# Kernel optimization log

Hardware: AMD Instinct MI355X
Metric: run time of the kernel (lower is better)

Reference implementation:

```python
import jax, jax.numpy as jnp
import numpy as np

NEG_INF = -1e10  # matches torch -10000000000.0


def setup_inputs() -> dict:
    key = jax.random.key(0)
    ks = jax.random.split(key, 8)
    L, B, E, H, HID, A = 2048, 32, 512, 512, 512, 512
    input_data = jax.random.normal(ks[0], (L, B, E), dtype=jnp.float32)
    mask = jax.random.randint(ks[1], (L, B), 0, 2, dtype=jnp.int32)
    action_feature = jax.random.normal(ks[2], (B, A), dtype=jnp.float32)
    hidden_state = jax.random.normal(ks[3], (B, H), dtype=jnp.float32)
    state = jax.random.normal(ks[4], (B, H), dtype=jnp.float32)
    W1 = jax.random.normal(ks[5], (H + E, HID), dtype=jnp.float32) * (1.0 / np.sqrt(H + E))
    b1 = jnp.zeros((HID,), dtype=jnp.float32)
    W2 = jax.random.normal(ks[6], (HID, 1), dtype=jnp.float32) * (1.0 / np.sqrt(HID))
    b2 = jnp.zeros((1,), dtype=jnp.float32)
    return {"input_data": input_data, "mask": mask, "action_feature": action_feature,
            "hidden_state": hidden_state, "state": state,
            "W1": W1, "b1": b1, "W2": W2, "b2": b2}


def reference(input_data, mask, action_feature, hidden_state, state, W1, b1, W2, b2):
    # input_data: (L, B, E); hidden_state: (B, H)
    H = hidden_state.shape[-1]
    # query = concat([hidden broadcast over L, input_data], -1); split W1 to avoid
    # materializing the (L, B, H+E) concat.
    W1_h, W1_e = W1[:H], W1[H:]                      # (H, HID), (E, HID)
    pre = hidden_state @ W1_h + b1                   # (B, HID)
    pre = pre[None] + jnp.einsum('lbe,eh->lbh', input_data, W1_e)  # (L, B, HID)
    logit = (jnp.tanh(pre) @ W2).squeeze(-1) + b2[0]  # (L, B)
    logit = jnp.where(mask != 0, logit, NEG_INF)
    p = jax.nn.softmax(logit, axis=0)                 # softmax over L
    ctx = jnp.einsum('lbe,lb->be', input_data, p)     # (B, E)
    return jnp.concatenate([ctx, action_feature], axis=1)
```

## Files before the change

### kernel.cpp

```cpp
#include <hip/hip_runtime.h>
#include <hip/hip_bf16.h>
#include <stdint.h>

#define L_DIM 2048
#define B_DIM 32
#define E_DIM 512
#define HID_DIM 512
#define M_DIM (L_DIM * B_DIM)

typedef float f32x4 __attribute__((ext_vector_type(4)));
typedef short bf16x8 __attribute__((ext_vector_type(8)));

#define OFF_BASE  0
#define OFF_WT    65536
#define OFF_LOGIT 589824
#define OFF_P     851968
#define OFF_PART  1114112

__device__ __forceinline__ unsigned short f2bf(float f) {
  unsigned int u = __float_as_uint(f);
  u = (u + 0x7FFFu + ((u >> 16) & 1u)) >> 16;
  return (unsigned short)u;
}

__device__ __forceinline__ float tanh_fast(float x) {
  float xc = fminf(fmaxf(x, -15.f), 15.f);
  float e = __expf(2.f * xc);
  return (e - 1.f) * __builtin_amdgcn_rcpf(e + 1.f);
}

__global__ __launch_bounds__(256) void k_base(const float* __restrict__ hidden,
                                              const float* __restrict__ W1,
                                              const float* __restrict__ b1,
                                              float* __restrict__ base) {
  const int b = blockIdx.x;
  const int tid = threadIdx.x;
  __shared__ float hs[HID_DIM];
  {
    float2 v = *(const float2*)(hidden + (size_t)b * 512 + tid * 2);
    hs[tid * 2] = v.x; hs[tid * 2 + 1] = v.y;
  }
  __syncthreads();
  const int h = tid * 2;
  float2 b1v = *(const float2*)(b1 + h);
  float ax = b1v.x, ay = b1v.y;
#pragma unroll 8
  for (int e = 0; e < 512; ++e) {
    float2 w = *(const float2*)(W1 + (size_t)e * 512 + h);
    float hv = hs[e];
    ax = fmaf(hv, w.x, ax);
    ay = fmaf(hv, w.y, ay);
  }
  float2 r; r.x = ax; r.y = ay;
  *(float2*)(base + (size_t)b * 512 + h) = r;
}

__global__ __launch_bounds__(256) void k_prep_wt(const float* __restrict__ W1,
                                                 unsigned short* __restrict__ Wt) {
  const int kc = blockIdx.x;
  const int tid = threadIdx.x;
  __shared__ unsigned short sh[32][516];
#pragma unroll
  for (int i = 0; i < 16; ++i) {
    int f4 = i * 256 + tid;
    int r = f4 >> 7;
    int c = (f4 & 127) * 4;
    float4 v = *(const float4*)(W1 + (size_t)(512 + kc * 32 + r) * 512 + c);
    sh[r][c + 0] = f2bf(v.x); sh[r][c + 1] = f2bf(v.y);
    sh[r][c + 2] = f2bf(v.z); sh[r][c + 3] = f2bf(v.w);
  }
  __syncthreads();
#pragma unroll
  for (int i = 0; i < 8; ++i) {
    int u = i * 256 + tid;
    int n = ((u >> 9) << 7) + (((u >> 6) & 7) << 4) + (u & 15);
    int k0 = ((u >> 4) & 3) << 3;
    alignas(16) unsigned short tmp[8];
#pragma unroll
    for (int j = 0; j < 8; ++j) tmp[j] = sh[k0 + j][n];
    *(uint4*)(Wt + ((size_t)kc * 2048 + u) * 8) = *(const uint4*)tmp;
  }
}

__global__ __launch_bounds__(512, 4) void k_logits(
    const float* __restrict__ x, const unsigned short* __restrict__ Wt,
    const float* __restrict__ base, const float* __restrict__ W2,
    float* __restrict__ logit) {
  __shared__ unsigned short xs[2][2048];
  const int tid = threadIdx.x;
  const int m0 = blockIdx.x * 64;
  const int w = tid >> 6, lane = tid & 63;
  const int lg = lane >> 4, l15 = lane & 15;

  const int row = tid >> 3, seg4 = tid & 7;
  const int seg8 = seg4 >> 1, half = seg4 & 1;
  const float* xsrc = x + (size_t)(m0 + row) * 512 + seg4 * 4;
  const int xsu = ((row >> 4) * 64 + seg8 * 16 + (row & 15)) * 8 + half * 4;

  int ub[4];
#pragma unroll
  for (int ni = 0; ni < 4; ++ni) {
    int nb = w * 64 + ni * 16;
    ub[ni] = ((nb >> 7) << 9) + (((nb >> 4) & 7) << 6);
  }

  {
    float4 v = *(const float4*)xsrc;
    uint2 pk;
    pk.x = (unsigned)f2bf(v.x) | ((unsigned)f2bf(v.y) << 16);
    pk.y = (unsigned)f2bf(v.z) | ((unsigned)f2bf(v.w) << 16);
    *(uint2*)(&xs[0][xsu]) = pk;
  }
  __syncthreads();

  f32x4 acc[4][4];
#pragma unroll
  for (int mi = 0; mi < 4; ++mi)
#pragma unroll
    for (int ni = 0; ni < 4; ++ni) acc[mi][ni] = (f32x4){0.f, 0.f, 0.f, 0.f};

  for (int kc = 0; kc < 16; ++kc) {
    const int cur = kc & 1;
    uint4 bw[4];
    const uint4* bsrc = (const uint4*)Wt + (size_t)kc * 2048;
#pragma unroll
    for (int ni = 0; ni < 4; ++ni) bw[ni] = bsrc[ub[ni] + lane];
    float4 nx;
    if (kc < 15) nx = *(const float4*)(xsrc + (kc + 1) * 32);
    bf16x8 af[4];
#pragma unroll
    for (int mi = 0; mi < 4; ++mi)
      af[mi] = *(const bf16x8*)(&xs[cur][(mi * 64 + lane) * 8]);
#pragma unroll
    for (int mi = 0; mi < 4; ++mi)
#pragma unroll
      for (int ni = 0; ni < 4; ++ni)
        acc[mi][ni] = __builtin_amdgcn_mfma_f32_16x16x32_bf16(
            af[mi], *(const bf16x8*)(&bw[ni]), acc[mi][ni], 0, 0, 0);
    if (kc < 15) {
      uint2 pk;
      pk.x = (unsigned)f2bf(nx.x) | ((unsigned)f2bf(nx.y) << 16);
      pk.y = (unsigned)f2bf(nx.z) | ((unsigned)f2bf(nx.w) << 16);
      *(uint2*)(&xs[cur ^ 1][xsu]) = pk;
    }
    __syncthreads();
  }

  float w2v[4];
#pragma unroll
  for (int ni = 0; ni < 4; ++ni) w2v[ni] = W2[w * 64 + ni * 16 + l15];
  float lsum[4][4];
#pragma unroll
  for (int mi = 0; mi < 4; ++mi) {
#pragma unroll
    for (int rg = 0; rg < 4; ++rg) {
      int m = m0 + mi * 16 + lg * 4 + rg;
      int bb = m & 31;
      const float* brow = base + (size_t)bb * 512 + w * 64;
      float s = 0.f;
#pragma unroll
      for (int ni = 0; ni < 4; ++ni) {
        float pre = acc[mi][ni][rg] + brow[ni * 16 + l15];
        s = fmaf(tanh_fast(pre), w2v[ni], s);
      }
      lsum[mi][rg] = s;
    }
  }
  float (*lred)[64] = (float (*)[64])xs;
#pragma unroll
  for (int mi = 0; mi < 4; ++mi)
#pragma unroll
    for (int rg = 0; rg < 4; ++rg) {
      float v = lsum[mi][rg];
      v += __shfl_xor(v, 1); v += __shfl_xor(v, 2);
      v += __shfl_xor(v, 4); v += __shfl_xor(v, 8);
      if (l15 == 0) lred[w][mi * 16 + lg * 4 + rg] = v;
    }
  __syncthreads();
  if (tid < 64) {
    float v = 0.f;
#pragma unroll
    for (int wq = 0; wq < 8; ++wq) v += lred[wq][tid];
    logit[m0 + tid] = v;
  }
}

__global__ __launch_bounds__(256) void k_softmax(const float* __restrict__ logit,
                                                 const int* __restrict__ mask,
                                                 float* __restrict__ p) {
  const int b = blockIdx.x, tid = threadIdx.x;
  float lv[8]; float mx = -3.0e38f;
#pragma unroll
  for (int i = 0; i < 8; ++i) {
    int idx = (tid + i * 256) * 32 + b;
    float v = (mask[idx] != 0) ? logit[idx] : -1.0e10f;
    lv[i] = v; mx = fmaxf(mx, v);
  }
  __shared__ float red[8];
  for (int d = 1; d < 64; d <<= 1) mx = fmaxf(mx, __shfl_xor(mx, d));
  if ((tid & 63) == 0) red[tid >> 6] = mx;
  __syncthreads();
  mx = fmaxf(fmaxf(red[0], red[1]), fmaxf(red[2], red[3]));
  float s = 0.f;
#pragma unroll
  for (int i = 0; i < 8; ++i) { lv[i] = __expf(lv[i] - mx); s += lv[i]; }
  for (int d = 1; d < 64; d <<= 1) s += __shfl_xor(s, d);
  __syncthreads();
  if ((tid & 63) == 0) red[4 + (tid >> 6)] = s;
  __syncthreads();
  s = (red[4] + red[5]) + (red[6] + red[7]);
  float inv = 1.f / s;
#pragma unroll
  for (int i = 0; i < 8; ++i) {
    int idx = (tid + i * 256) * 32 + b;
    p[idx] = lv[i] * inv;
  }
}

__global__ __launch_bounds__(128) void k_ctx(const float* __restrict__ x,
                                             const float* __restrict__ p,
                                             float* __restrict__ part) {
  const int blk = blockIdx.x;
  const int b = blk >> 5, ch = blk & 31;
  const int tid = threadIdx.x;
  __shared__ float ps[64];
  const int l0 = ch * 64;
  if (tid < 64) ps[tid] = p[(l0 + tid) * 32 + b];
  __syncthreads();
  const float* xb = x + ((size_t)l0 * 32 + b) * 512 + tid * 4;
  float ax = 0.f, ay = 0.f, az = 0.f, aw = 0.f;
#pragma unroll 4
  for (int i = 0; i < 64; ++i) {
    float4 v = *(const float4*)(xb + (size_t)i * 32 * 512);
    float pv = ps[i];
    ax = fmaf(pv, v.x, ax); ay = fmaf(pv, v.y, ay);
    az = fmaf(pv, v.z, az); aw = fmaf(pv, v.w, aw);
  }
  float4 r; r.x = ax; r.y = ay; r.z = az; r.w = aw;
  *(float4*)(part + (size_t)blk * 512 + tid * 4) = r;
}

__global__ __launch_bounds__(256) void k_final(const float* __restrict__ part,
                                               const float* __restrict__ af,
                                               float* __restrict__ out) {
  const int b = blockIdx.x, tid = threadIdx.x;
  float ax = 0.f, ay = 0.f;
#pragma unroll
  for (int ch = 0; ch < 32; ++ch) {
    float2 v = *(const float2*)(part + ((size_t)(b * 32 + ch) * 512) + tid * 2);
    ax += v.x; ay += v.y;
  }
  float2 r; r.x = ax; r.y = ay;
  *(float2*)(out + (size_t)b * 1024 + tid * 2) = r;
  float2 a = *(const float2*)(af + (size_t)b * 512 + tid * 2);
  *(float2*)(out + (size_t)b * 1024 + 512 + tid * 2) = a;
}

extern "C" void kernel_launch(void* const* d_in, const int* in_sizes, int n_in,
                              void* d_out, int out_size, void* d_ws, size_t ws_size,
                              hipStream_t stream) {
  const float* x      = (const float*)d_in[0];
  const int*   mask   = (const int*)d_in[1];
  const float* af     = (const float*)d_in[2];
  const float* hidden = (const float*)d_in[3];
  const float* W1     = (const float*)d_in[5];
  const float* b1     = (const float*)d_in[6];
  const float* W2     = (const float*)d_in[7];
  float* out = (float*)d_out;
  char* ws = (char*)d_ws;
  float*          base  = (float*)(ws + OFF_BASE);
  unsigned short* Wt    = (unsigned short*)(ws + OFF_WT);
  float*          logit = (float*)(ws + OFF_LOGIT);
  float*          p     = (float*)(ws + OFF_P);
  float*          part  = (float*)(ws + OFF_PART);

  k_base   <<<32,   256, 0, stream>>>(hidden, W1, b1, base);
  k_prep_wt<<<16,   256, 0, stream>>>(W1, Wt);
  k_logits <<<1024, 512, 0, stream>>>(x, Wt, base, W2, logit);
  k_softmax<<<32,   256, 0, stream>>>(logit, mask, p);
  k_ctx    <<<1024, 128, 0, stream>>>(x, p, part);
  k_final  <<<32,   256, 0, stream>>>(part, af, out);
}
```

Before: 107.3 us.

## Stage full 64x512 X tile in LDS up front, drop per-k-step barriers

k_logits now loads and converts the block's entire 64-row X tile to bf16 into 64KB of shared memory before the K loop, instead of double-buffering one 32-wide K chunk per iteration. The K loop then needs no __syncthreads and is unrolled by 2, so MFMA work runs without a block barrier every step. In exchange LDS use per block rises from 8KB to 64KB, which limits how many blocks fit per CU (the launch bounds ask for 4), and global load latency is no longer hidden behind compute. A barrier is added before the shared buffer is reused for the reduction.

```diff
diff --git a/kernel.cpp b/kernel.cpp
--- a/kernel.cpp
+++ b/kernel.cpp
@@ -27,6 +27,15 @@
   float xc = fminf(fmaxf(x, -15.f), 15.f);
   float e = __expf(2.f * xc);
   return (e - 1.f) * __builtin_amdgcn_rcpf(e + 1.f);
+}
+
+__device__ __forceinline__ uint4 pack8(const float4& a, const float4& b) {
+  uint4 r;
+  r.x = (unsigned)f2bf(a.x) | ((unsigned)f2bf(a.y) << 16);
+  r.y = (unsigned)f2bf(a.z) | ((unsigned)f2bf(a.w) << 16);
+  r.z = (unsigned)f2bf(b.x) | ((unsigned)f2bf(b.y) << 16);
+  r.w = (unsigned)f2bf(b.z) | ((unsigned)f2bf(b.w) << 16);
+  return r;
 }
 
 __global__ __launch_bounds__(256) void k_base(const float* __restrict__ hidden,
@@ -86,16 +95,26 @@
     const float* __restrict__ x, const unsigned short* __restrict__ Wt,
     const float* __restrict__ base, const float* __restrict__ W2,
     float* __restrict__ logit) {
-  __shared__ unsigned short xs[2][2048];
+  __shared__ unsigned short xs[32768];
   const int tid = threadIdx.x;
   const int m0 = blockIdx.x * 64;
   const int w = tid >> 6, lane = tid & 63;
   const int lg = lane >> 4, l15 = lane & 15;
 
-  const int row = tid >> 3, seg4 = tid & 7;
-  const int seg8 = seg4 >> 1, half = seg4 & 1;
-  const float* xsrc = x + (size_t)(m0 + row) * 512 + seg4 * 4;
-  const int xsu = ((row >> 4) * 64 + seg8 * 16 + (row & 15)) * 8 + half * 4;
+  {
+    const int r = tid >> 3, j = tid & 7;
+    const float* xrow = x + (size_t)(m0 + r) * 512;
+    const int ubase = ((r >> 4) << 6) + (r & 15);
+#pragma unroll
+    for (int i = 0; i < 8; ++i) {
+      int s = i * 8 + j;
+      float4 a0 = *(const float4*)(xrow + s * 8);
+      float4 a1 = *(const float4*)(xrow + s * 8 + 4);
+      int u = ((s >> 2) << 8) + ((s & 3) << 4) + ubase;
+      *(uint4*)(&xs[u * 8]) = pack8(a0, a1);
+    }
+  }
+  __syncthreads();
 
   int ub[4];
 #pragma unroll
@@ -104,46 +123,28 @@
     ub[ni] = ((nb >> 7) << 9) + (((nb >> 4) & 7) << 6);
   }
 
-  {
-    float4 v = *(const float4*)xsrc;
-    uint2 pk;
-    pk.x = (unsigned)f2bf(v.x) | ((unsigned)f2bf(v.y) << 16);
-    pk.y = (unsigned)f2bf(v.z) | ((unsigned)f2bf(v.w) << 16);
-    *(uint2*)(&xs[0][xsu]) = pk;
-  }
-  __syncthreads();
-
   f32x4 acc[4][4];
 #pragma unroll
   for (int mi = 0; mi < 4; ++mi)
 #pragma unroll
     for (int ni = 0; ni < 4; ++ni) acc[mi][ni] = (f32x4){0.f, 0.f, 0.f, 0.f};
 
+#pragma unroll 2
   for (int kc = 0; kc < 16; ++kc) {
-    const int cur = kc & 1;
     uint4 bw[4];
     const uint4* bsrc = (const uint4*)Wt + (size_t)kc * 2048;
 #pragma unroll
     for (int ni = 0; ni < 4; ++ni) bw[ni] = bsrc[ub[ni] + lane];
-    float4 nx;
-    if (kc < 15) nx = *(const float4*)(xsrc + (kc + 1) * 32);
     bf16x8 af[4];
 #pragma unroll
     for (int mi = 0; mi < 4; ++mi)
-      af[mi] = *(const bf16x8*)(&xs[cur][(mi * 64 + lane) * 8]);
+      af[mi] = *(const bf16x8*)(&xs[(kc * 256 + mi * 64 + lane) * 8]);
 #pragma unroll
     for (int mi = 0; mi < 4; ++mi)
 #pragma unroll
       for (int ni = 0; ni < 4; ++ni)
         acc[mi][ni] = __builtin_amdgcn_mfma_f32_16x16x32_bf16(
             af[mi], *(const bf16x8*)(&bw[ni]), acc[mi][ni], 0, 0, 0);
-    if (kc < 15) {
-      uint2 pk;
-      pk.x = (unsigned)f2bf(nx.x) | ((unsigned)f2bf(nx.y) << 16);
-      pk.y = (unsigned)f2bf(nx.z) | ((unsigned)f2bf(nx.w) << 16);
-      *(uint2*)(&xs[cur ^ 1][xsu]) = pk;
-    }
-    __syncthreads();
   }
 
   float w2v[4];
@@ -166,6 +167,7 @@
       lsum[mi][rg] = s;
     }
   }
+  __syncthreads();
   float (*lred)[64] = (float (*)[64])xs;
 #pragma unroll
   for (int mi = 0; mi < 4; ++mi)
```

Result: slower. 111.3 us (+3.7%).

## Double the logits tile to 128 rows and software-pipeline weight loads

Applied to the files above, without the earlier changes.

The logits GEMM kernel now uses 1024-thread blocks covering 128 rows. Two row groups of waves share each weight fragment load, halving weight traffic per row. Weight fragments are prefetched one k-step ahead into registers through inline global_load asm with explicit vmcnt waits, and the MFMA section runs at raised wave priority. The larger tile and extra prefetch registers raise register pressure under launch_bounds(1024,4), which may cause spills or lower occupancy.

```diff
diff --git a/kernel.cpp b/kernel.cpp
--- a/kernel.cpp
+++ b/kernel.cpp
@@ -10,6 +10,7 @@
 
 typedef float f32x4 __attribute__((ext_vector_type(4)));
 typedef short bf16x8 __attribute__((ext_vector_type(8)));
+typedef unsigned int u32x4 __attribute__((ext_vector_type(4)));
 
 #define OFF_BASE  0
 #define OFF_WT    65536
@@ -28,6 +29,12 @@
   float e = __expf(2.f * xc);
   return (e - 1.f) * __builtin_amdgcn_rcpf(e + 1.f);
 }
+
+#define GLX4(dst, voff, sbase) \
+  asm volatile("global_load_dwordx4 %0, %1, %2" \
+               : "=v"(dst) : "v"(voff), "s"(sbase))
+#define VMWAIT(N) do { asm volatile("s_waitcnt vmcnt(" #N ")" ::: "memory"); \
+                       __builtin_amdgcn_sched_barrier(0); } while (0)
 
 __global__ __launch_bounds__(256) void k_base(const float* __restrict__ hidden,
                                               const float* __restrict__ W1,
@@ -82,81 +89,116 @@
   }
 }
 
-__global__ __launch_bounds__(512, 4) void k_logits(
+__global__ __launch_bounds__(1024, 4) void k_logits(
     const float* __restrict__ x, const unsigned short* __restrict__ Wt,
     const float* __restrict__ base, const float* __restrict__ W2,
     float* __restrict__ logit) {
-  __shared__ unsigned short xs[2][2048];
+  __shared__ unsigned short xs[2][4096];
+  __shared__ float lred[2][8][64];
   const int tid = threadIdx.x;
-  const int m0 = blockIdx.x * 64;
+  const int m0 = blockIdx.x * 128;
   const int w = tid >> 6, lane = tid & 63;
+  const int wm = w >> 3, wn = w & 7;
   const int lg = lane >> 4, l15 = lane & 15;
 
-  const int row = tid >> 3, seg4 = tid & 7;
-  const int seg8 = seg4 >> 1, half = seg4 & 1;
-  const float* xsrc = x + (size_t)(m0 + row) * 512 + seg4 * 4;
-  const int xsu = ((row >> 4) * 64 + seg8 * 16 + (row & 15)) * 8 + half * 4;
-
-  int ub[4];
-#pragma unroll
-  for (int ni = 0; ni < 4; ++ni) {
-    int nb = w * 64 + ni * 16;
-    ub[ni] = ((nb >> 7) << 9) + (((nb >> 4) & 7) << 6);
-  }
+  const int xr = tid >> 3, xseg = tid & 7;
+  const float* xsrc = x + (size_t)(m0 + xr) * 512 + xseg * 4;
+  const int xu8 = (((xr >> 4) << 6) + ((xseg >> 1) << 4) + (xr & 15)) * 8 +
+                  (xseg & 1) * 4;
+
+  unsigned vo[4];
+#pragma unroll
+  for (int ni = 0; ni < 4; ++ni)
+    vo[ni] = ((unsigned)((wn >> 1) * 512 + ((wn & 1) * 4 + ni) * 64 + lane)) * 16u;
+
+  f32x4 acc[4][4];
+#pragma unroll
+  for (int mi = 0; mi < 4; ++mi)
+#pragma unroll
+    for (int ni = 0; ni < 4; ++ni) acc[mi][ni] = (f32x4){0.f, 0.f, 0.f, 0.f};
 
   {
     float4 v = *(const float4*)xsrc;
     uint2 pk;
     pk.x = (unsigned)f2bf(v.x) | ((unsigned)f2bf(v.y) << 16);
     pk.y = (unsigned)f2bf(v.z) | ((unsigned)f2bf(v.w) << 16);
-    *(uint2*)(&xs[0][xsu]) = pk;
-  }
-  __syncthreads();
-
-  f32x4 acc[4][4];
-#pragma unroll
-  for (int mi = 0; mi < 4; ++mi)
-#pragma unroll
-    for (int ni = 0; ni < 4; ++ni) acc[mi][ni] = (f32x4){0.f, 0.f, 0.f, 0.f};
-
-  for (int kc = 0; kc < 16; ++kc) {
+    *(uint2*)(&xs[0][xu8]) = pk;
+  }
+  u32x4 bw[4];
+#pragma unroll
+  for (int ni = 0; ni < 4; ++ni) { GLX4(bw[ni], vo[ni], Wt); vo[ni] += 32768u; }
+  __syncthreads();
+
+#pragma unroll 1
+  for (int kc = 0; kc < 15; ++kc) {
     const int cur = kc & 1;
-    uint4 bw[4];
-    const uint4* bsrc = (const uint4*)Wt + (size_t)kc * 2048;
-#pragma unroll
-    for (int ni = 0; ni < 4; ++ni) bw[ni] = bsrc[ub[ni] + lane];
     float4 nx;
-    if (kc < 15) nx = *(const float4*)(xsrc + (kc + 1) * 32);
+    {
+      unsigned long long xp = (unsigned long long)(xsrc + (kc + 1) * 32);
+      asm volatile("" : "+v"(xp));
+      nx = *(const float4*)xp;
+    }
+    u32x4 bn[4];
+#pragma unroll
+    for (int ni = 0; ni < 4; ++ni) { GLX4(bn[ni], vo[ni], Wt); vo[ni] += 32768u; }
     bf16x8 af[4];
 #pragma unroll
     for (int mi = 0; mi < 4; ++mi)
-      af[mi] = *(const bf16x8*)(&xs[cur][(mi * 64 + lane) * 8]);
+      af[mi] = *(const bf16x8*)(&xs[cur][((wm * 4 + mi) * 64 + lane) * 8]);
+    VMWAIT(5);
+    asm volatile("s_waitcnt lgkmcnt(0)" ::: "memory");
+    __builtin_amdgcn_sched_barrier(0);
+    __builtin_amdgcn_s_setprio(1);
 #pragma unroll
     for (int mi = 0; mi < 4; ++mi)
 #pragma unroll
       for (int ni = 0; ni < 4; ++ni)
         acc[mi][ni] = __builtin_amdgcn_mfma_f32_16x16x32_bf16(
             af[mi], *(const bf16x8*)(&bw[ni]), acc[mi][ni], 0, 0, 0);
-    if (kc < 15) {
+    __builtin_amdgcn_s_setprio(0);
+    VMWAIT(4);
+    {
       uint2 pk;
       pk.x = (unsigned)f2bf(nx.x) | ((unsigned)f2bf(nx.y) << 16);
       pk.y = (unsigned)f2bf(nx.z) | ((unsigned)f2bf(nx.w) << 16);
-      *(uint2*)(&xs[cur ^ 1][xsu]) = pk;
+      *(uint2*)(&xs[cur ^ 1][xu8]) = pk;
     }
+#pragma unroll
+    for (int ni = 0; ni < 4; ++ni) bw[ni] = bn[ni];
     __syncthreads();
   }
-
+  {
+    bf16x8 af[4];
+#pragma unroll
+    for (int mi = 0; mi < 4; ++mi)
+      af[mi] = *(const bf16x8*)(&xs[1][((wm * 4 + mi) * 64 + lane) * 8]);
+    VMWAIT(0);
+    asm volatile("s_waitcnt lgkmcnt(0)" ::: "memory");
+    __builtin_amdgcn_sched_barrier(0);
+#pragma unroll
+    for (int mi = 0; mi < 4; ++mi)
+#pragma unroll
+      for (int ni = 0; ni < 4; ++ni)
+        acc[mi][ni] = __builtin_amdgcn_mfma_f32_16x16x32_bf16(
+            af[mi], *(const bf16x8*)(&bw[ni]), acc[mi][ni], 0, 0, 0);
+  }
+
+  unsigned long long bpi = (unsigned long long)base;
+  unsigned long long wpi = (unsigned long long)W2;
+  asm volatile("" : "+s"(bpi), "+s"(wpi));
+  const float* bp = (const float*)bpi;
+  const float* wp = (const float*)wpi;
   float w2v[4];
 #pragma unroll
-  for (int ni = 0; ni < 4; ++ni) w2v[ni] = W2[w * 64 + ni * 16 + l15];
+  for (int ni = 0; ni < 4; ++ni) w2v[ni] = wp[wn * 64 + ni * 16 + l15];
   float lsum[4][4];
 #pragma unroll
   for (int mi = 0; mi < 4; ++mi) {
 #pragma unroll
     for (int rg = 0; rg < 4; ++rg) {
-      int m = m0 + mi * 16 + lg * 4 + rg;
+      int m = m0 + wm * 64 + mi * 16 + lg * 4 + rg;
       int bb = m & 31;
-      const float* brow = base + (size_t)bb * 512 + w * 64;
+      const float* brow = bp + (size_t)bb * 512 + wn * 64;
       float s = 0.f;
 #pragma unroll
       for (int ni = 0; ni < 4; ++ni) {
@@ -166,7 +208,6 @@
       lsum[mi][rg] = s;
     }
   }
-  float (*lred)[64] = (float (*)[64])xs;
 #pragma unroll
   for (int mi = 0; mi < 4; ++mi)
 #pragma unroll
@@ -174,13 +215,14 @@
       float v = lsum[mi][rg];
       v += __shfl_xor(v, 1); v += __shfl_xor(v, 2);
       v += __shfl_xor(v, 4); v += __shfl_xor(v, 8);
-      if (l15 == 0) lred[w][mi * 16 + lg * 4 + rg] = v;
+      if (l15 == 0) lred[wm][wn][mi * 16 + lg * 4 + rg] = v;
     }
   __syncthreads();
-  if (tid < 64) {
+  if (tid < 128) {
+    const int wmr = tid >> 6, row = tid & 63;
     float v = 0.f;
 #pragma unroll
-    for (int wq = 0; wq < 8; ++wq) v += lred[wq][tid];
+    for (int wq = 0; wq < 8; ++wq) v += lred[wmr][wq][row];
     logit[m0 + tid] = v;
   }
 }
@@ -276,7 +318,7 @@
 
   k_base   <<<32,   256, 0, stream>>>(hidden, W1, b1, base);
   k_prep_wt<<<16,   256, 0, stream>>>(W1, Wt);
-  k_logits <<<1024, 512, 0, stream>>>(x, Wt, base, W2, logit);
+  k_logits <<<512, 1024, 0, stream>>>(x, Wt, base, W2, logit);
   k_softmax<<<32,   256, 0, stream>>>(logit, mask, p);
   k_ctx    <<<1024, 128, 0, stream>>>(x, p, part);
   k_final  <<<32,   256, 0, stream>>>(part, af, out);
```

Measured after the change: 114.3 us. 6.6% more time.

## Stage W1 tiles through double-buffered LDS via async global_load_lds

Applied to the files above, without the earlier changes.

Weight fragments were previously loaded straight from global memory into registers each k-step. Now each block prefetches the next k-chunk of the transposed weight into a double-buffered LDS region using global_load_lds, overlapped with the MFMA work on the current chunk. MFMA sections are also wrapped in s_setprio to favor the math waves. The cost is 64KB of extra LDS per block, which may lower occupancy below the 4-blocks launch bound and reduce latency hiding.

```diff
diff --git a/kernel.cpp b/kernel.cpp
--- a/kernel.cpp
+++ b/kernel.cpp
@@ -28,6 +28,11 @@
   float e = __expf(2.f * xc);
   return (e - 1.f) * __builtin_amdgcn_rcpf(e + 1.f);
 }
+
+#define GLOAD_LDS16(gsrc, ldst) \
+  __builtin_amdgcn_global_load_lds( \
+      (const __attribute__((address_space(1))) void*)(gsrc), \
+      (__attribute__((address_space(3))) void*)(ldst), 16, 0, 0)
 
 __global__ __launch_bounds__(256) void k_base(const float* __restrict__ hidden,
                                               const float* __restrict__ W1,
@@ -86,62 +91,78 @@
     const float* __restrict__ x, const unsigned short* __restrict__ Wt,
     const float* __restrict__ base, const float* __restrict__ W2,
     float* __restrict__ logit) {
-  __shared__ unsigned short xs[2][2048];
+  __shared__ unsigned short bs[2][16384];
+  __shared__ unsigned short xsh[2][2048];
   const int tid = threadIdx.x;
   const int m0 = blockIdx.x * 64;
   const int w = tid >> 6, lane = tid & 63;
   const int lg = lane >> 4, l15 = lane & 15;
 
-  const int row = tid >> 3, seg4 = tid & 7;
-  const int seg8 = seg4 >> 1, half = seg4 & 1;
-  const float* xsrc = x + (size_t)(m0 + row) * 512 + seg4 * 4;
-  const int xsu = ((row >> 4) * 64 + seg8 * 16 + (row & 15)) * 8 + half * 4;
+  const int xr = tid >> 3, xseg = tid & 7;
+  const float* xsrc = x + (size_t)(m0 + xr) * 512 + xseg * 4;
+  const int xu8 = (((xr >> 4) << 6) + ((xseg >> 1) << 4) + (xr & 15)) * 8 +
+                  (xseg & 1) * 4;
 
   int ub[4];
 #pragma unroll
   for (int ni = 0; ni < 4; ++ni) {
-    int nb = w * 64 + ni * 16;
-    ub[ni] = ((nb >> 7) << 9) + (((nb >> 4) & 7) << 6);
-  }
-
+    int q = 4 * w + ni;
+    ub[ni] = (q >> 3) * 512 + (q & 7) * 64;
+  }
+
+  f32x4 acc[4][4];
+#pragma unroll
+  for (int mi = 0; mi < 4; ++mi)
+#pragma unroll
+    for (int ni = 0; ni < 4; ++ni) acc[mi][ni] = (f32x4){0.f, 0.f, 0.f, 0.f};
+
+#pragma unroll
+  for (int j = 0; j < 4; ++j) {
+    const int cu = j * 512 + w * 64;
+    GLOAD_LDS16(Wt + (size_t)(cu + lane) * 8, &bs[0][cu * 8]);
+  }
   {
     float4 v = *(const float4*)xsrc;
     uint2 pk;
     pk.x = (unsigned)f2bf(v.x) | ((unsigned)f2bf(v.y) << 16);
     pk.y = (unsigned)f2bf(v.z) | ((unsigned)f2bf(v.w) << 16);
-    *(uint2*)(&xs[0][xsu]) = pk;
-  }
-  __syncthreads();
-
-  f32x4 acc[4][4];
-#pragma unroll
-  for (int mi = 0; mi < 4; ++mi)
-#pragma unroll
-    for (int ni = 0; ni < 4; ++ni) acc[mi][ni] = (f32x4){0.f, 0.f, 0.f, 0.f};
-
+    *(uint2*)(&xsh[0][xu8]) = pk;
+  }
+  __syncthreads();
+
+#pragma unroll 1
   for (int kc = 0; kc < 16; ++kc) {
-    const int cur = kc & 1;
-    uint4 bw[4];
-    const uint4* bsrc = (const uint4*)Wt + (size_t)kc * 2048;
-#pragma unroll
-    for (int ni = 0; ni < 4; ++ni) bw[ni] = bsrc[ub[ni] + lane];
+    const int cur = kc & 1, nxt = cur ^ 1;
     float4 nx;
-    if (kc < 15) nx = *(const float4*)(xsrc + (kc + 1) * 32);
-    bf16x8 af[4];
+    if (kc < 15) {
+      const unsigned short* wsrc = Wt + (size_t)(kc + 1) * 16384;
+#pragma unroll
+      for (int j = 0; j < 4; ++j) {
+        const int cu = j * 512 + w * 64;
+        GLOAD_LDS16(wsrc + (size_t)(cu + lane) * 8, &bs[nxt][cu * 8]);
+      }
+      nx = *(const float4*)(xsrc + (kc + 1) * 32);
+    }
+    bf16x8 af[4], bf[4];
 #pragma unroll
     for (int mi = 0; mi < 4; ++mi)
-      af[mi] = *(const bf16x8*)(&xs[cur][(mi * 64 + lane) * 8]);
+      af[mi] = *(const bf16x8*)(&xsh[cur][(mi * 64 + lane) * 8]);
+#pragma unroll
+    for (int ni = 0; ni < 4; ++ni)
+      bf[ni] = *(const bf16x8*)(&bs[cur][(ub[ni] + lane) * 8]);
+    __builtin_amdgcn_s_setprio(1);
 #pragma unroll
     for (int mi = 0; mi < 4; ++mi)
 #pragma unroll
       for (int ni = 0; ni < 4; ++ni)
         acc[mi][ni] = __builtin_amdgcn_mfma_f32_16x16x32_bf16(
-            af[mi], *(const bf16x8*)(&bw[ni]), acc[mi][ni], 0, 0, 0);
+            af[mi], bf[ni], acc[mi][ni], 0, 0, 0);
+    __builtin_amdgcn_s_setprio(0);
     if (kc < 15) {
       uint2 pk;
       pk.x = (unsigned)f2bf(nx.x) | ((unsigned)f2bf(nx.y) << 16);
       pk.y = (unsigned)f2bf(nx.z) | ((unsigned)f2bf(nx.w) << 16);
-      *(uint2*)(&xs[cur ^ 1][xsu]) = pk;
+      *(uint2*)(&xsh[nxt][xu8]) = pk;
     }
     __syncthreads();
   }
@@ -166,7 +187,7 @@
       lsum[mi][rg] = s;
     }
   }
-  float (*lred)[64] = (float (*)[64])xs;
+  float (*lred)[64] = (float (*)[64])xsh;
 #pragma unroll
   for (int mi = 0; mi < 4; ++mi)
 #pragma unroll
```

Measured after the change: 120.7 us. +12.5%, slower.
